# Kernel optimization log

Hardware: AMD Instinct MI355X
Metric: run time of the kernel (lower is better)

## Reference

```python
import jax, jax.numpy as jnp
import numpy as np

B = 4096
FEATURES = 4608 + 4608 + 8 + 1  # 9225
LSTM = 512
R = FEATURES / LSTM
D1 = int(FEATURES / R ** (1.0 / 3.0))
D2 = int(FEATURES / R ** (2.0 / 3.0))
ACTION_SHAPES = (64, 64, 64, 64, 64, 64, 64, 64)


def setup_inputs() -> dict:
    key = jax.random.key(0)
    ks = jax.random.split(key, 32)
    s = 0.02
    inp = {
        "actualCanvasFeatures": jax.random.normal(ks[0], (B, 4608), jnp.float32),
        "objectiveCanvasFeatures": jax.random.normal(ks[1], (B, 4608), jnp.float32),
        "last_action": jax.random.uniform(ks[2], (B, 8), jnp.float32),
        "episode_percentage": 0,
        # encoder MLP
        "W1": jax.random.normal(ks[3], (FEATURES, D1), jnp.float32) * s,
        "b1": jnp.zeros((D1,), jnp.float32),
        "W2": jax.random.normal(ks[4], (D1, D2), jnp.float32) * s,
        "b2": jnp.zeros((D2,), jnp.float32),
        "W3": jax.random.normal(ks[5], (D2, LSTM), jnp.float32) * s,
        "b3": jnp.zeros((LSTM,), jnp.float32),
        # LSTM (torch gate order i,f,g,o)
        "Wih": jax.random.normal(ks[6], (4 * LSTM, LSTM), jnp.float32) * s,
        "Whh": jax.random.normal(ks[7], (4 * LSTM, LSTM), jnp.float32) * s,
        "bih": jnp.zeros((4 * LSTM,), jnp.float32),
        "bhh": jnp.zeros((4 * LSTM,), jnp.float32),
        "h0": jnp.zeros((B, LSTM), jnp.float32),
        "c0": jnp.zeros((B, LSTM), jnp.float32),
        # decoder
        "dW1": jax.random.normal(ks[8], (LSTM, LSTM // 2), jnp.float32) * s,
        "db1": jnp.zeros((LSTM // 2,), jnp.float32),
        "headWs": tuple(jax.random.normal(ks[9 + i], (LSTM // 2, a), jnp.float32) * s
                        for i, a in enumerate(ACTION_SHAPES)),
        "headbs": tuple(jnp.zeros((a,), jnp.float32) for a in ACTION_SHAPES),
        "dWo": jax.random.normal(ks[20], (LSTM + 1, LSTM), jnp.float32) * s,
        "dbo": jnp.zeros((LSTM,), jnp.float32),
    }
    return inp


def reference(actualCanvasFeatures, objectiveCanvasFeatures, last_action,
              episode_percentage, W1, b1, W2, b2, W3, b3, Wih, Whh, bih, bhh,
              h0, c0, dW1, db1, headWs, headbs, dWo, dbo):
    b = actualCanvasFeatures.shape[0]
    ep = jnp.full((b, 1), episode_percentage, dtype=jnp.float32)
    feats = jnp.concatenate(
        [actualCanvasFeatures, objectiveCanvasFeatures, last_action, ep], axis=1)
    # encoder MLP (dropout is eval-mode identity)
    x = jax.nn.relu(feats @ W1 + b1)
    x = jax.nn.relu(x @ W2 + b2)
    x = jax.nn.relu(x @ W3 + b3)
    # single-step LSTM cell, torch gate order i,f,g,o
    gates = x @ Wih.T + bih + h0 @ Whh.T + bhh
    i, f, g, o = jnp.split(gates, 4, axis=1)
    c = jax.nn.sigmoid(f) * c0 + jax.nn.sigmoid(i) * jnp.tanh(g)
    z = jax.nn.sigmoid(o) * jnp.tanh(c)  # seed
    key = jax.random.key(42)
    actions = []
    log_probabilities = jnp.zeros((b,), jnp.float32)
    entropy = jnp.float32(0.0)
    for Wk, bk in zip(headWs, headbs):
        z1 = jax.nn.relu(z @ dW1 + db1)
        logits = z1 @ Wk + bk
        logp = jax.nn.log_softmax(logits, axis=1)
        probs = jnp.exp(logp)
        key, sk = jax.random.split(key)
        act = jax.random.categorical(sk, logits, axis=1)  # [b] int
        actions.append(act.astype(jnp.float32))
        entropy = entropy + jnp.sum(-jnp.sum(probs * logp, axis=1))
        log_probabilities = log_probabilities + jnp.take_along_axis(
            logp, act[:, None], axis=1)[:, 0]
        z = jax.nn.relu(
            jnp.concatenate([z, act.astype(jnp.float32)[:, None]], axis=1) @ dWo + dbo)
    action = jnp.stack(actions, axis=1)  # [b, n_sub_actions]
    return action, entropy, log_probabilities
```

## Files before the change

kernel.cpp:

```cpp
#include <hip/hip_runtime.h>
#include <cstdint>
#include <cstring>

typedef _Float16 f16;
typedef _Float16 f16x8 __attribute__((ext_vector_type(8)));
typedef float f32x4 __attribute__((ext_vector_type(4)));

static constexpr int kPartitionable = 1;

__host__ __device__ inline void tf2x32(uint32_t k0, uint32_t k1,
                                       uint32_t x0, uint32_t x1,
                                       uint32_t& o0, uint32_t& o1) {
  uint32_t ks[3] = {k0, k1, k0 ^ k1 ^ 0x1BD11BDAu};
  uint32_t v0 = x0 + ks[0], v1 = x1 + ks[1];
  const int r0[4] = {13, 15, 26, 6};
  const int r1[4] = {17, 29, 16, 24};
  for (int g = 0; g < 5; ++g) {
    const int* rr = (g & 1) ? r1 : r0;
    for (int j = 0; j < 4; ++j) {
      v0 += v1;
      v1 = (v1 << rr[j]) | (v1 >> (32 - rr[j]));
      v1 ^= v0;
    }
    v0 += ks[(g + 1) % 3];
    v1 += ks[(g + 2) % 3] + (uint32_t)(g + 1);
  }
  o0 = v0; o1 = v1;
}

template <int BM, int BN>
__global__ __launch_bounds__(256, 2) void gemm_split(
    const f16* __restrict__ Ah, const f16* __restrict__ Al, int lda,
    const f16* __restrict__ Bh, const f16* __restrict__ Bl, int ldb,
    int K,
    const float* __restrict__ bias1, const float* __restrict__ bias2,
    int nReal, int relu, int writeF32,
    float* __restrict__ outF, f16* __restrict__ outH, f16* __restrict__ outL,
    int ldo) {
  constexpr int BK = 64;
  constexpr int BKP = BK + 8;
  constexpr int TM = BM / 32;
  constexpr int TN = BN / 32;
  static_assert(BM == BN, "square tiles only");
  __shared__ f16 sAh[BM * BKP];
  __shared__ f16 sAl[BM * BKP];
  __shared__ f16 sBh[BN * BKP];
  __shared__ f16 sBl[BN * BKP];

  const int tid = threadIdx.x;
  const int wave = tid >> 6;
  const int lane = tid & 63;
  const int wm = wave & 1, wn = wave >> 1;
  const int m0 = blockIdx.x * BM;
  const int n0 = blockIdx.y * BN;

  f32x4 acc[TM][TN];
  const f32x4 zero = {0.f, 0.f, 0.f, 0.f};
#pragma unroll
  for (int i = 0; i < TM; ++i)
#pragma unroll
    for (int j = 0; j < TN; ++j) acc[i][j] = zero;

  const f16* src;
  f16* dst;
  int ld, base;
  if (wave == 0)      { src = Ah; dst = sAh; ld = lda; base = m0; }
  else if (wave == 1) { src = Al; dst = sAl; ld = lda; base = m0; }
  else if (wave == 2) { src = Bh; dst = sBh; ld = ldb; base = n0; }
  else                { src = Bl; dst = sBl; ld = ldb; base = n0; }
  constexpr int NITER = (BM * 8) / 64;

  for (int k0 = 0; k0 < K; k0 += BK) {
    __syncthreads();
#pragma unroll
    for (int j = 0; j < NITER; ++j) {
      int c = j * 64 + lane;
      int row = c >> 3, col = c & 7;
      const uint4* g = (const uint4*)(src + (size_t)(base + row) * ld + k0) + col;
      uint4 v = *g;
      ((uint4*)dst)[row * 9 + col] = v;
    }
    __syncthreads();
#pragma unroll
    for (int kk = 0; kk < BK; kk += 32) {
      const int fr = lane & 15;
      const int q8 = (lane >> 4) * 8;
      f16x8 aH[TM], aL[TM], bH[TN], bL[TN];
#pragma unroll
      for (int i = 0; i < TM; ++i) {
        int off = (wm * (BM / 2) + i * 16 + fr) * BKP + kk + q8;
        aH[i] = *(const f16x8*)&sAh[off];
        aL[i] = *(const f16x8*)&sAl[off];
      }
#pragma unroll
      for (int j = 0; j < TN; ++j) {
        int off = (wn * (BN / 2) + j * 16 + fr) * BKP + kk + q8;
        bH[j] = *(const f16x8*)&sBh[off];
        bL[j] = *(const f16x8*)&sBl[off];
      }
#pragma unroll
      for (int i = 0; i < TM; ++i)
#pragma unroll
        for (int j = 0; j < TN; ++j) {
          acc[i][j] = __builtin_amdgcn_mfma_f32_16x16x32_f16(aH[i], bH[j], acc[i][j], 0, 0, 0);
          acc[i][j] = __builtin_amdgcn_mfma_f32_16x16x32_f16(aH[i], bL[j], acc[i][j], 0, 0, 0);
          acc[i][j] = __builtin_amdgcn_mfma_f32_16x16x32_f16(aL[i], bH[j], acc[i][j], 0, 0, 0);
        }
    }
  }
  const int rq = lane >> 4, cl = lane & 15;
#pragma unroll
  for (int i = 0; i < TM; ++i)
#pragma unroll
    for (int j = 0; j < TN; ++j)
#pragma unroll
      for (int r = 0; r < 4; ++r) {
        int row = m0 + wm * (BM / 2) + i * 16 + rq * 4 + r;
        int col = n0 + wn * (BN / 2) + j * 16 + cl;
        float v = acc[i][j][r];
        if (col < nReal) {
          if (bias1) v += bias1[col];
          if (bias2) v += bias2[col];
          if (relu) v = fmaxf(v, 0.f);
        } else {
          v = 0.f;
        }
        size_t o = (size_t)row * ldo + col;
        if (writeF32) {
          outF[o] = v;
        } else {
          f16 h = (f16)v;
          outH[o] = h;
          outL[o] = (f16)(v - (float)h);
        }
      }
}

__global__ void conv_feats(const float* __restrict__ A, const float* __restrict__ O,
                           const float* __restrict__ LA, const int* __restrict__ EP,
                           f16* __restrict__ H, f16* __restrict__ L) {
  uint32_t idx = blockIdx.x * 256u + threadIdx.x;
  const uint32_t total = 4096u * 9280u;
  if (idx >= total) return;
  uint32_t b = idx / 9280u, c = idx - b * 9280u;
  float v;
  if (c < 4608u) v = A[(size_t)b * 4608 + c];
  else if (c < 9216u) v = O[(size_t)b * 4608 + (c - 4608u)];
  else if (c < 9224u) v = LA[(size_t)b * 8 + (c - 9216u)];
  else if (c == 9224u) v = (float)EP[0];
  else v = 0.f;
  f16 h = (f16)v;
  H[idx] = h;
  L[idx] = (f16)(v - (float)h);
}

__global__ void convT_kernel(const float* __restrict__ W, int Kreal, int Nreal,
                             f16* __restrict__ BtH, f16* __restrict__ BtL, int Kpad) {
  __shared__ float tile[32][33];
  int k0 = blockIdx.x * 32, n0 = blockIdx.y * 32;
  int tx = threadIdx.x, ty = threadIdx.y;
  for (int r = 0; r < 32; r += 8) {
    int k = k0 + ty + r, n = n0 + tx;
    float v = (k < Kreal && n < Nreal) ? W[(size_t)k * Nreal + n] : 0.f;
    tile[ty + r][tx] = v;
  }
  __syncthreads();
  for (int r = 0; r < 32; r += 8) {
    int n = n0 + ty + r, k = k0 + tx;
    float v = tile[tx][ty + r];
    size_t o = (size_t)n * Kpad + k;
    f16 h = (f16)v;
    BtH[o] = h;
    BtL[o] = (f16)(v - (float)h);
  }
}

__global__ void conv_lstmB(const float* __restrict__ Wih, const float* __restrict__ Whh,
                           f16* __restrict__ H, f16* __restrict__ L) {
  uint32_t idx = blockIdx.x * 256u + threadIdx.x;
  uint32_t n = idx >> 10, k = idx & 1023u;
  float v = (k < 512u) ? Wih[(size_t)n * 512 + k] : Whh[(size_t)n * 512 + (k - 512u)];
  f16 h = (f16)v;
  H[idx] = h;
  L[idx] = (f16)(v - (float)h);
}

__global__ void conv_h0(const float* __restrict__ h0, f16* __restrict__ H, f16* __restrict__ L) {
  uint32_t idx = blockIdx.x * 256u + threadIdx.x;
  uint32_t b = idx >> 9, j = idx & 511u;
  float v = h0[idx];
  size_t o = (size_t)b * 1024 + 512 + j;
  f16 h = (f16)v;
  H[o] = h;
  L[o] = (f16)(v - (float)h);
}

__global__ void lstm_pointwise(const float* __restrict__ gates, const float* __restrict__ c0,
                               f16* __restrict__ zH, f16* __restrict__ zL) {
  uint32_t idx = blockIdx.x * 256u + threadIdx.x;
  uint32_t b = idx >> 9, n = idx & 511u;
  const float* g = gates + (size_t)b * 2048;
  float gi = g[n], gf = g[512 + n], gg = g[1024 + n], go = g[1536 + n];
  float si = 1.f / (1.f + expf(-gi));
  float sf = 1.f / (1.f + expf(-gf));
  float so = 1.f / (1.f + expf(-go));
  float c = sf * c0[idx] + si * tanhf(gg);
  float z = so * tanhf(c);
  size_t o = (size_t)b * 576 + n;
  f16 h = (f16)z;
  zH[o] = h;
  zL[o] = (f16)(z - (float)h);
}

__global__ void init_ws(f16* zAH, f16* zAL, f16* zBH, f16* zBL,
                        float* wsLogp, float* wsEnt) {
  uint32_t idx = blockIdx.x * 256u + threadIdx.x;
  if (idx < 4096u * 63u) {
    uint32_t b = idx / 63u, c = 513u + idx - b * 63u;
    size_t o = (size_t)b * 576 + c;
    zAH[o] = (f16)0.f; zAL[o] = (f16)0.f; zBH[o] = (f16)0.f; zBL[o] = (f16)0.f;
  }
  if (idx < 4096u) wsLogp[idx] = 0.f;
  if (idx == 0) *wsEnt = 0.f;
}

__device__ inline double shfl_xor_dbl(double v, int m) {
  union { double d; int i[2]; } u;
  u.d = v;
  u.i[0] = __shfl_xor(u.i[0], m);
  u.i[1] = __shfl_xor(u.i[1], m);
  return u.d;
}

__global__ void sample_head(const float* __restrict__ logits,
                            uint32_t sk0, uint32_t sk1, int head, int partitionable,
                            float* __restrict__ outAct,
                            f16* __restrict__ zH, f16* __restrict__ zL,
                            float* __restrict__ wsLogp, float* __restrict__ wsEnt) {
  int wave = threadIdx.x >> 6, lane = threadIdx.x & 63;
  int b = blockIdx.x * 4 + wave;
  float l = logits[(size_t)b * 128 + lane];

  uint32_t i = (uint32_t)b * 64u + (uint32_t)lane;
  uint32_t bits;
  if (partitionable) {
    uint32_t o0, o1;
    tf2x32(sk0, sk1, 0u, i, o0, o1);
    bits = o0 ^ o1;
  } else {
    const uint32_t H = 131072u;
    uint32_t c0, c1, o0, o1;
    int pick;
    if (i < H) { c0 = i; c1 = i + H; pick = 0; }
    else       { c0 = i - H; c1 = i; pick = 1; }
    tf2x32(sk0, sk1, c0, c1, o0, o1);
    bits = pick ? o1 : o0;
  }
  uint32_t ub = (bits >> 9) | 0x3f800000u;
  float u;
  __builtin_memcpy(&u, &ub, 4);
  u -= 1.0f;
  if (u == 0.0f) u = 1.17549435e-38f;
  double gum = -log(-log((double)u));
  double s = (double)l + gum;

  int bi = lane;
  double bv = s;
#pragma unroll
  for (int off = 1; off < 64; off <<= 1) {
    double ov = shfl_xor_dbl(bv, off);
    int oi = __shfl_xor(bi, off);
    if (ov > bv || (ov == bv && oi < bi)) { bv = ov; bi = oi; }
  }
  int act = bi;

  float m = l;
#pragma unroll
  for (int off = 1; off < 64; off <<= 1) m = fmaxf(m, __shfl_xor(m, off));
  float e = expf(l - m);
  float S = e, D = e * l;
#pragma unroll
  for (int off = 1; off < 64; off <<= 1) {
    S += __shfl_xor(S, off);
    D += __shfl_xor(D, off);
  }
  float M = m + logf(S);
  float Hrow = M - D / S;
  float l_act = __shfl(l, act);

  if (lane == 0) {
    outAct[(size_t)b * 8 + head] = (float)act;
    wsLogp[b] += (l_act - M);
    size_t zo = (size_t)b * 576 + 512;
    zH[zo] = (f16)act;
    zL[zo] = (f16)0.f;
  }
  __shared__ float hs[4];
  if (lane == 0) hs[wave] = Hrow;
  __syncthreads();
  if (threadIdx.x == 0) atomicAdd(wsEnt, hs[0] + hs[1] + hs[2] + hs[3]);
}

__global__ void finalize_out(const float* __restrict__ wsEnt, const float* __restrict__ wsLogp,
                             float* __restrict__ out) {
  uint32_t idx = blockIdx.x * 256u + threadIdx.x;
  if (idx == 0) out[32768] = *wsEnt;
  if (idx < 4096u) out[32769 + idx] = wsLogp[idx];
}

extern "C" void kernel_launch(void* const* d_in, const int* in_sizes, int n_in,
                              void* d_out, int out_size, void* d_ws, size_t ws_size,
                              hipStream_t stream) {
  (void)in_sizes; (void)out_size; (void)ws_size;
  const float* actual = (const float*)d_in[0];
  const float* object = (const float*)d_in[1];
  const float* lastA = (const float*)d_in[2];
  const int* ep = (const int*)d_in[3];
  const float* W1 = (const float*)d_in[4];
  const float* b1 = (const float*)d_in[5];
  const float* W2 = (const float*)d_in[6];
  const float* b2 = (const float*)d_in[7];
  const float* W3 = (const float*)d_in[8];
  const float* b3 = (const float*)d_in[9];
  const float* Wih = (const float*)d_in[10];
  const float* Whh = (const float*)d_in[11];
  const float* bih = (const float*)d_in[12];
  const float* bhh = (const float*)d_in[13];
  const float* h0 = (const float*)d_in[14];
  const float* c0 = (const float*)d_in[15];
  const float* dW1 = (const float*)d_in[16];
  const float* db1 = (const float*)d_in[17];
  const float* headW[8];
  const float* headb[8];
  const float *dWo, *dbo;
  if (n_in >= 36) {
    for (int h = 0; h < 8; ++h) headW[h] = (const float*)d_in[18 + h];
    for (int h = 0; h < 8; ++h) headb[h] = (const float*)d_in[26 + h];
    dWo = (const float*)d_in[34];
    dbo = (const float*)d_in[35];
  } else {
    const float* hw = (const float*)d_in[18];
    const float* hb = (const float*)d_in[19];
    for (int h = 0; h < 8; ++h) { headW[h] = hw + (size_t)h * 256 * 64; headb[h] = hb + (size_t)h * 64; }
    dWo = (const float*)d_in[20];
    dbo = (const float*)d_in[21];
  }

  constexpr int Bq = 4096;
  constexpr int K1 = 9280, N1 = 3584, N1r = 3518;
  constexpr int K2 = 3584, N2 = 1408, N2r = 1342;
  constexpr int K3 = 1408, N3 = 512;
  constexpr int KL = 1024, NL = 2048;
  constexpr int KD1 = 512, ND1 = 256;
  constexpr int KH = 256, NHp = 128;
  constexpr int KDO = 576, NDO = 512;

  uint8_t* w = (uint8_t*)d_ws;
  size_t off = 0;
  auto alloc = [&](size_t bytes) -> void* {
    off = (off + 1023) & ~(size_t)1023;
    void* p = w + off;
    off += bytes;
    return p;
  };
  f16* A1h = (f16*)alloc((size_t)Bq * K1 * 2);
  f16* A1l = (f16*)alloc((size_t)Bq * K1 * 2);
  size_t fixedReuseEnd = off;
  f16* Bt1h = (f16*)alloc((size_t)N1 * K1 * 2);
  f16* Bt1l = (f16*)alloc((size_t)N1 * K1 * 2);
  f16* x1h = (f16*)alloc((size_t)Bq * K2 * 2);
  f16* x1l = (f16*)alloc((size_t)Bq * K2 * 2);
  f16* Bt2h = (f16*)alloc((size_t)N2 * K2 * 2);
  f16* Bt2l = (f16*)alloc((size_t)N2 * K2 * 2);
  size_t poff = 0;
  auto palloc = [&](size_t bytes) -> void* {
    poff = (poff + 1023) & ~(size_t)1023;
    void* p = w + poff;
    poff += bytes;
    return p;
  };
  f16* x2h = (f16*)palloc((size_t)Bq * K3 * 2);
  f16* x2l = (f16*)palloc((size_t)Bq * K3 * 2);
  f16* Bt3h = (f16*)palloc((size_t)N3 * K3 * 2);
  f16* Bt3l = (f16*)palloc((size_t)N3 * K3 * 2);
  f16* ALh = (f16*)palloc((size_t)Bq * KL * 2);
  f16* ALl = (f16*)palloc((size_t)Bq * KL * 2);
  f16* BLh = (f16*)palloc((size_t)NL * KL * 2);
  f16* BLl = (f16*)palloc((size_t)NL * KL * 2);
  float* gates = (float*)palloc((size_t)Bq * NL * 4);
  f16* zAH = (f16*)palloc((size_t)Bq * 576 * 2);
  f16* zAL = (f16*)palloc((size_t)Bq * 576 * 2);
  f16* zBH = (f16*)palloc((size_t)Bq * 576 * 2);
  f16* zBL = (f16*)palloc((size_t)Bq * 576 * 2);
  f16* Btd1h = (f16*)palloc((size_t)ND1 * KD1 * 2);
  f16* Btd1l = (f16*)palloc((size_t)ND1 * KD1 * 2);
  f16* z1h = (f16*)palloc((size_t)Bq * ND1 * 2);
  f16* z1l = (f16*)palloc((size_t)Bq * ND1 * 2);
  f16* Bthh = (f16*)palloc((size_t)8 * NHp * KH * 2);
  f16* Bthl = (f16*)palloc((size_t)8 * NHp * KH * 2);
  float* logitsF = (float*)palloc((size_t)Bq * 128 * 4);
  f16* Btdoh = (f16*)palloc((size_t)NDO * KDO * 2);
  f16* Btdol = (f16*)palloc((size_t)NDO * KDO * 2);
  float* wsLogp = (float*)palloc((size_t)Bq * 4);
  float* wsEnt = (float*)palloc(64);
  (void)fixedReuseEnd;

  uint32_t k0 = 0u, k1 = 42u;
  uint32_t sk[8][2];
  for (int h = 0; h < 8; ++h) {
    if (kPartitionable) {
      uint32_t a0, a1, b0v, b1v;
      tf2x32(k0, k1, 0u, 0u, a0, a1);
      tf2x32(k0, k1, 0u, 1u, b0v, b1v);
      sk[h][0] = b0v; sk[h][1] = b1v;
      k0 = a0; k1 = a1;
    } else {
      uint32_t a0, a1, b0v, b1v;
      tf2x32(k0, k1, 0u, 2u, a0, a1);
      tf2x32(k0, k1, 1u, 3u, b0v, b1v);
      sk[h][0] = a1; sk[h][1] = b1v;
      k0 = a0; k1 = b0v;
    }
  }

  dim3 blk(256);
  dim3 tblk(32, 8);

  conv_feats<<<(4096u * 9280u + 255) / 256, blk, 0, stream>>>(actual, object, lastA, ep, A1h, A1l);
  convT_kernel<<<dim3(K1 / 32, N1 / 32), tblk, 0, stream>>>(W1, 9225, 3518, Bt1h, Bt1l, K1);
  convT_kernel<<<dim3(K2 / 32, N2 / 32), tblk, 0, stream>>>(W2, 3518, 1342, Bt2h, Bt2l, K2);

  gemm_split<128, 128><<<dim3(Bq / 128, N1 / 128), blk, 0, stream>>>(
      A1h, A1l, K1, Bt1h, Bt1l, K1, K1, b1, nullptr, N1r, 1, 0, nullptr, x1h, x1l, K2);

  init_ws<<<(4096u * 63u + 255) / 256, blk, 0, stream>>>(zAH, zAL, zBH, zBL, wsLogp, wsEnt);
  convT_kernel<<<dim3(K3 / 32, N3 / 32), tblk, 0, stream>>>(W3, 1342, 512, Bt3h, Bt3l, K3);
  conv_lstmB<<<(2048u * 1024u) / 256, blk, 0, stream>>>(Wih, Whh, BLh, BLl);
  conv_h0<<<(4096u * 512u) / 256, blk, 0, stream>>>(h0, ALh, ALl);
  convT_kernel<<<dim3(KD1 / 32, ND1 / 32), tblk, 0, stream>>>(dW1, 512, 256, Btd1h, Btd1l, KD1);
  convT_kernel<<<dim3(KDO / 32, NDO / 32), tblk, 0, stream>>>(dWo, 513, 512, Btdoh, Btdol, KDO);
  for (int h = 0; h < 8; ++h)
    convT_kernel<<<dim3(KH / 32, NHp / 32), tblk, 0, stream>>>(
        headW[h], 256, 64, Bthh + (size_t)h * NHp * KH, Bthl + (size_t)h * NHp * KH, KH);

  gemm_split<128, 128><<<dim3(Bq / 128, N2 / 128), blk, 0, stream>>>(
      x1h, x1l, K2, Bt2h, Bt2l, K2, K2, b2, nullptr, N2r, 1, 0, nullptr, x2h, x2l, K3);
  gemm_split<128, 128><<<dim3(Bq / 128, N3 / 128), blk, 0, stream>>>(
      x2h, x2l, K3, Bt3h, Bt3l, K3, K3, b3, nullptr, N3, 1, 0, nullptr, ALh, ALl, KL);
  gemm_split<128, 128><<<dim3(Bq / 128, NL / 128), blk, 0, stream>>>(
      ALh, ALl, KL, BLh, BLl, KL, KL, bih, bhh, NL, 0, 1, gates, nullptr, nullptr, NL);
  lstm_pointwise<<<(4096u * 512u) / 256, blk, 0, stream>>>(gates, c0, zAH, zAL);

  for (int h = 0; h < 8; ++h) {
    f16* curH = (h & 1) ? zBH : zAH;
    f16* curL = (h & 1) ? zBL : zAL;
    f16* nxtH = (h & 1) ? zAH : zBH;
    f16* nxtL = (h & 1) ? zAL : zBL;
    gemm_split<64, 64><<<dim3(Bq / 64, ND1 / 64), blk, 0, stream>>>(
        curH, curL, 576, Btd1h, Btd1l, KD1, KD1, db1, nullptr, ND1, 1, 0, nullptr, z1h, z1l, ND1);
    gemm_split<64, 64><<<dim3(Bq / 64, NHp / 64), blk, 0, stream>>>(
        z1h, z1l, ND1, Bthh + (size_t)h * NHp * KH, Bthl + (size_t)h * NHp * KH, KH, KH,
        headb[h], nullptr, 64, 0, 1, logitsF, nullptr, nullptr, 128);
    sample_head<<<Bq / 4, blk, 0, stream>>>(logitsF, sk[h][0], sk[h][1], h, kPartitionable,
                                            (float*)d_out, curH, curL, wsLogp, wsEnt);
    gemm_split<64, 64><<<dim3(Bq / 64, NDO / 64), blk, 0, stream>>>(
        curH, curL, 576, Btdoh, Btdol, KDO, KDO, dbo, nullptr, NDO, 1, 0, nullptr, nxtH, nxtL, 576);
  }
  finalize_out<<<(4097 + 255) / 256, blk, 0, stream>>>(wsEnt, wsLogp, (float*)d_out);
}
```

Before: 2.024 ms.

## Fuse autoregressive decoder loop into one persistent kernel with LDS-resident state

Replaces the 8-head decoder loop of 32 separate GEMM and sampling launches plus finalize with a single kernel, where each 16-row block keeps z, z1 and logits in shared memory across all heads. It also merges the eight head-weight transposes into one launch and drops the workspace init and finalize kernels. The aim is to remove launch overhead and global round-trips for the intermediate activations. The cost is that only 256 blocks run, each with small 16-row MFMA tiles that read weights directly from global memory without LDS staging, so the kernel may be latency-bound and have low occupancy.

```diff
diff --git a/kernel.cpp b/kernel.cpp
--- a/kernel.cpp
+++ b/kernel.cpp
@@ -7,6 +7,9 @@
 typedef float f32x4 __attribute__((ext_vector_type(4)));
 
 static constexpr int kPartitionable = 1;
+
+struct Ptr8 { const float* p[8]; };
+struct Keys8 { uint32_t k[8][2]; };
 
 __host__ __device__ inline void tf2x32(uint32_t k0, uint32_t k1,
                                        uint32_t x0, uint32_t x1,
@@ -175,6 +178,29 @@
   }
 }
 
+__global__ void convT_heads(Ptr8 ws, f16* __restrict__ BtH, f16* __restrict__ BtL) {
+  __shared__ float tile[32][33];
+  int h = blockIdx.z;
+  const float* W = ws.p[h];
+  int k0 = blockIdx.x * 32, n0 = blockIdx.y * 32;
+  int tx = threadIdx.x, ty = threadIdx.y;
+  for (int r = 0; r < 32; r += 8) {
+    int k = k0 + ty + r, n = n0 + tx;
+    float v = (k < 256 && n < 64) ? W[(size_t)k * 64 + n] : 0.f;
+    tile[ty + r][tx] = v;
+  }
+  __syncthreads();
+  size_t base = (size_t)h * 64 * 256;
+  for (int r = 0; r < 32; r += 8) {
+    int n = n0 + ty + r, k = k0 + tx;
+    float v = tile[tx][ty + r];
+    size_t o = base + (size_t)n * 256 + k;
+    f16 hh = (f16)v;
+    BtH[o] = hh;
+    BtL[o] = (f16)(v - (float)hh);
+  }
+}
+
 __global__ void conv_lstmB(const float* __restrict__ Wih, const float* __restrict__ Whh,
                            f16* __restrict__ H, f16* __restrict__ L) {
   uint32_t idx = blockIdx.x * 256u + threadIdx.x;
@@ -206,22 +232,13 @@
   float so = 1.f / (1.f + expf(-go));
   float c = sf * c0[idx] + si * tanhf(gg);
   float z = so * tanhf(c);
-  size_t o = (size_t)b * 576 + n;
   f16 h = (f16)z;
-  zH[o] = h;
-  zL[o] = (f16)(z - (float)h);
-}
-
-__global__ void init_ws(f16* zAH, f16* zAL, f16* zBH, f16* zBL,
-                        float* wsLogp, float* wsEnt) {
-  uint32_t idx = blockIdx.x * 256u + threadIdx.x;
-  if (idx < 4096u * 63u) {
-    uint32_t b = idx / 63u, c = 513u + idx - b * 63u;
-    size_t o = (size_t)b * 576 + c;
-    zAH[o] = (f16)0.f; zAL[o] = (f16)0.f; zBH[o] = (f16)0.f; zBL[o] = (f16)0.f;
-  }
-  if (idx < 4096u) wsLogp[idx] = 0.f;
-  if (idx == 0) *wsEnt = 0.f;
+  zH[idx] = h;
+  zL[idx] = (f16)(z - (float)h);
+}
+
+__global__ void init_ent(float* __restrict__ out) {
+  if (threadIdx.x == 0 && blockIdx.x == 0) out[32768] = 0.f;
 }
 
 __device__ inline double shfl_xor_dbl(double v, int m) {
@@ -232,80 +249,194 @@
   return u.d;
 }
 
-__global__ void sample_head(const float* __restrict__ logits,
-                            uint32_t sk0, uint32_t sk1, int head, int partitionable,
-                            float* __restrict__ outAct,
-                            f16* __restrict__ zH, f16* __restrict__ zL,
-                            float* __restrict__ wsLogp, float* __restrict__ wsEnt) {
-  int wave = threadIdx.x >> 6, lane = threadIdx.x & 63;
-  int b = blockIdx.x * 4 + wave;
-  float l = logits[(size_t)b * 128 + lane];
-
-  uint32_t i = (uint32_t)b * 64u + (uint32_t)lane;
-  uint32_t bits;
-  if (partitionable) {
-    uint32_t o0, o1;
-    tf2x32(sk0, sk1, 0u, i, o0, o1);
-    bits = o0 ^ o1;
-  } else {
-    const uint32_t H = 131072u;
-    uint32_t c0, c1, o0, o1;
-    int pick;
-    if (i < H) { c0 = i; c1 = i + H; pick = 0; }
-    else       { c0 = i - H; c1 = i; pick = 1; }
-    tf2x32(sk0, sk1, c0, c1, o0, o1);
-    bits = pick ? o1 : o0;
-  }
-  uint32_t ub = (bits >> 9) | 0x3f800000u;
-  float u;
-  __builtin_memcpy(&u, &ub, 4);
-  u -= 1.0f;
-  if (u == 0.0f) u = 1.17549435e-38f;
-  double gum = -log(-log((double)u));
-  double s = (double)l + gum;
-
-  int bi = lane;
-  double bv = s;
-#pragma unroll
-  for (int off = 1; off < 64; off <<= 1) {
-    double ov = shfl_xor_dbl(bv, off);
-    int oi = __shfl_xor(bi, off);
-    if (ov > bv || (ov == bv && oi < bi)) { bv = ov; bi = oi; }
-  }
-  int act = bi;
-
-  float m = l;
-#pragma unroll
-  for (int off = 1; off < 64; off <<= 1) m = fmaxf(m, __shfl_xor(m, off));
-  float e = expf(l - m);
-  float S = e, D = e * l;
-#pragma unroll
-  for (int off = 1; off < 64; off <<= 1) {
-    S += __shfl_xor(S, off);
-    D += __shfl_xor(D, off);
-  }
-  float M = m + logf(S);
-  float Hrow = M - D / S;
-  float l_act = __shfl(l, act);
-
-  if (lane == 0) {
-    outAct[(size_t)b * 8 + head] = (float)act;
-    wsLogp[b] += (l_act - M);
-    size_t zo = (size_t)b * 576 + 512;
-    zH[zo] = (f16)act;
-    zL[zo] = (f16)0.f;
-  }
-  __shared__ float hs[4];
-  if (lane == 0) hs[wave] = Hrow;
+__global__ __launch_bounds__(256, 2) void decoder_fused(
+    const f16* __restrict__ zH0, const f16* __restrict__ zL0,
+    const f16* __restrict__ Bd1H, const f16* __restrict__ Bd1L,
+    const float* __restrict__ db1,
+    const f16* __restrict__ BhH, const f16* __restrict__ BhL,
+    Ptr8 hb,
+    const f16* __restrict__ BdoH, const f16* __restrict__ BdoL,
+    const float* __restrict__ dbo,
+    Keys8 sk, int partitionable,
+    float* __restrict__ out) {
+  constexpr int ZS = 584;
+  constexpr int Z1S = 264;
+  __shared__ f16 zbH[16 * ZS], zbL[16 * ZS];
+  __shared__ f16 z1H[16 * Z1S], z1L[16 * Z1S];
+  __shared__ float lgt[16 * 64];
+  __shared__ float entSh[4];
+
+  const int tid = threadIdx.x;
+  const int wave = tid >> 6, lane = tid & 63;
+  const int fr = lane & 15, rq = lane >> 4;
+  const int q8 = rq * 8;
+  const int rowG0 = blockIdx.x * 16;
+  const f32x4 zero = {0.f, 0.f, 0.f, 0.f};
+
+#pragma unroll
+  for (int t = 0; t < 4; ++t) {
+    int ch = t * 256 + tid;
+    int r = ch >> 6, c8 = (ch & 63) * 8;
+    *(f16x8*)&zbH[r * ZS + c8] = *(const f16x8*)&zH0[(size_t)(rowG0 + r) * 512 + c8];
+    *(f16x8*)&zbL[r * ZS + c8] = *(const f16x8*)&zL0[(size_t)(rowG0 + r) * 512 + c8];
+  }
+  if (tid < 128) {
+    int r = tid >> 3, c8 = 512 + (tid & 7) * 8;
+    f16x8 zz = {0, 0, 0, 0, 0, 0, 0, 0};
+    *(f16x8*)&zbH[r * ZS + c8] = zz;
+    *(f16x8*)&zbL[r * ZS + c8] = zz;
+  }
+
+  float entAcc = 0.f;
+  float logpAcc[4] = {0.f, 0.f, 0.f, 0.f};
+
+  for (int h = 0; h < 8; ++h) {
+    __syncthreads();
+    {
+      f32x4 acc[4];
+#pragma unroll
+      for (int j = 0; j < 4; ++j) acc[j] = zero;
+      for (int k0 = 0; k0 < 512; k0 += 32) {
+        f16x8 aH = *(const f16x8*)&zbH[fr * ZS + k0 + q8];
+        f16x8 aL = *(const f16x8*)&zbL[fr * ZS + k0 + q8];
+#pragma unroll
+        for (int j = 0; j < 4; ++j) {
+          int n = wave * 64 + j * 16 + fr;
+          f16x8 bH = *(const f16x8*)&Bd1H[n * 512 + k0 + q8];
+          f16x8 bL = *(const f16x8*)&Bd1L[n * 512 + k0 + q8];
+          acc[j] = __builtin_amdgcn_mfma_f32_16x16x32_f16(aH, bH, acc[j], 0, 0, 0);
+          acc[j] = __builtin_amdgcn_mfma_f32_16x16x32_f16(aH, bL, acc[j], 0, 0, 0);
+          acc[j] = __builtin_amdgcn_mfma_f32_16x16x32_f16(aL, bH, acc[j], 0, 0, 0);
+        }
+      }
+#pragma unroll
+      for (int j = 0; j < 4; ++j) {
+        int col = wave * 64 + j * 16 + fr;
+        float bb = db1[col];
+#pragma unroll
+        for (int r = 0; r < 4; ++r) {
+          float v = fmaxf(acc[j][r] + bb, 0.f);
+          int row = rq * 4 + r;
+          f16 hv = (f16)v;
+          z1H[row * Z1S + col] = hv;
+          z1L[row * Z1S + col] = (f16)(v - (float)hv);
+        }
+      }
+    }
+    __syncthreads();
+    {
+      f32x4 acc = zero;
+      const f16* BH = BhH + (size_t)h * 64 * 256;
+      const f16* BL = BhL + (size_t)h * 64 * 256;
+      int n = wave * 16 + fr;
+      for (int k0 = 0; k0 < 256; k0 += 32) {
+        f16x8 aH = *(const f16x8*)&z1H[fr * Z1S + k0 + q8];
+        f16x8 aL = *(const f16x8*)&z1L[fr * Z1S + k0 + q8];
+        f16x8 bH = *(const f16x8*)&BH[n * 256 + k0 + q8];
+        f16x8 bL = *(const f16x8*)&BL[n * 256 + k0 + q8];
+        acc = __builtin_amdgcn_mfma_f32_16x16x32_f16(aH, bH, acc, 0, 0, 0);
+        acc = __builtin_amdgcn_mfma_f32_16x16x32_f16(aH, bL, acc, 0, 0, 0);
+        acc = __builtin_amdgcn_mfma_f32_16x16x32_f16(aL, bH, acc, 0, 0, 0);
+      }
+      float bb = hb.p[h][n];
+#pragma unroll
+      for (int r = 0; r < 4; ++r) lgt[(rq * 4 + r) * 64 + n] = acc[r] + bb;
+    }
+    __syncthreads();
+    for (int rr = 0; rr < 4; ++rr) {
+      int row = wave * 4 + rr;
+      int b = rowG0 + row;
+      float l = lgt[row * 64 + lane];
+      uint32_t i = (uint32_t)b * 64u + (uint32_t)lane;
+      uint32_t bits;
+      if (partitionable) {
+        uint32_t o0, o1;
+        tf2x32(sk.k[h][0], sk.k[h][1], 0u, i, o0, o1);
+        bits = o0 ^ o1;
+      } else {
+        const uint32_t Hh = 131072u;
+        uint32_t c0, c1, o0, o1;
+        int pick;
+        if (i < Hh) { c0 = i; c1 = i + Hh; pick = 0; }
+        else        { c0 = i - Hh; c1 = i; pick = 1; }
+        tf2x32(sk.k[h][0], sk.k[h][1], c0, c1, o0, o1);
+        bits = pick ? o1 : o0;
+      }
+      uint32_t ub = (bits >> 9) | 0x3f800000u;
+      float u;
+      __builtin_memcpy(&u, &ub, 4);
+      u -= 1.0f;
+      if (u == 0.0f) u = 1.17549435e-38f;
+      double gum = -log(-log((double)u));
+      double s = (double)l + gum;
+      int bi = lane;
+      double bv = s;
+#pragma unroll
+      for (int off = 1; off < 64; off <<= 1) {
+        double ov = shfl_xor_dbl(bv, off);
+        int oi = __shfl_xor(bi, off);
+        if (ov > bv || (ov == bv && oi < bi)) { bv = ov; bi = oi; }
+      }
+      int act = bi;
+      float m = l;
+#pragma unroll
+      for (int off = 1; off < 64; off <<= 1) m = fmaxf(m, __shfl_xor(m, off));
+      float e = expf(l - m);
+      float S = e, D = e * l;
+#pragma unroll
+      for (int off = 1; off < 64; off <<= 1) {
+        S += __shfl_xor(S, off);
+        D += __shfl_xor(D, off);
+      }
+      float M = m + logf(S);
+      entAcc += (M - D / S);
+      float l_act = __shfl(l, act);
+      logpAcc[rr] += (l_act - M);
+      if (lane == 0) {
+        out[(size_t)b * 8 + h] = (float)act;
+        zbH[row * ZS + 512] = (f16)act;
+        zbL[row * ZS + 512] = (f16)0.f;
+      }
+    }
+    __syncthreads();
+    {
+      f32x4 accD[8];
+#pragma unroll
+      for (int j = 0; j < 8; ++j) accD[j] = zero;
+      for (int k0 = 0; k0 < 576; k0 += 32) {
+        f16x8 aH = *(const f16x8*)&zbH[fr * ZS + k0 + q8];
+        f16x8 aL = *(const f16x8*)&zbL[fr * ZS + k0 + q8];
+#pragma unroll
+        for (int j = 0; j < 8; ++j) {
+          int n = wave * 128 + j * 16 + fr;
+          f16x8 bH = *(const f16x8*)&BdoH[n * 576 + k0 + q8];
+          f16x8 bL = *(const f16x8*)&BdoL[n * 576 + k0 + q8];
+          accD[j] = __builtin_amdgcn_mfma_f32_16x16x32_f16(aH, bH, accD[j], 0, 0, 0);
+          accD[j] = __builtin_amdgcn_mfma_f32_16x16x32_f16(aH, bL, accD[j], 0, 0, 0);
+          accD[j] = __builtin_amdgcn_mfma_f32_16x16x32_f16(aL, bH, accD[j], 0, 0, 0);
+        }
+      }
+      __syncthreads();
+#pragma unroll
+      for (int j = 0; j < 8; ++j) {
+        int col = wave * 128 + j * 16 + fr;
+        float bb = dbo[col];
+#pragma unroll
+        for (int r = 0; r < 4; ++r) {
+          float v = fmaxf(accD[j][r] + bb, 0.f);
+          int row = rq * 4 + r;
+          f16 hv = (f16)v;
+          zbH[row * ZS + col] = hv;
+          zbL[row * ZS + col] = (f16)(v - (float)hv);
+        }
+      }
+    }
+  }
+  if (lane == 0) entSh[wave] = entAcc;
   __syncthreads();
-  if (threadIdx.x == 0) atomicAdd(wsEnt, hs[0] + hs[1] + hs[2] + hs[3]);
-}
-
-__global__ void finalize_out(const float* __restrict__ wsEnt, const float* __restrict__ wsLogp,
-                             float* __restrict__ out) {
-  uint32_t idx = blockIdx.x * 256u + threadIdx.x;
-  if (idx == 0) out[32768] = *wsEnt;
-  if (idx < 4096u) out[32769 + idx] = wsLogp[idx];
+  if (tid == 0) atomicAdd(&out[32768], entSh[0] + entSh[1] + entSh[2] + entSh[3]);
+  if (lane == 0)
+    for (int rr = 0; rr < 4; ++rr) out[32769 + rowG0 + wave * 4 + rr] = logpAcc[rr];
 }
 
 extern "C" void kernel_launch(void* const* d_in, const int* in_sizes, int n_in,
@@ -340,8 +471,8 @@
     dbo = (const float*)d_in[35];
   } else {
     const float* hw = (const float*)d_in[18];
-    const float* hb = (const float*)d_in[19];
-    for (int h = 0; h < 8; ++h) { headW[h] = hw + (size_t)h * 256 * 64; headb[h] = hb + (size_t)h * 64; }
+    const float* hbp = (const float*)d_in[19];
+    for (int h = 0; h < 8; ++h) { headW[h] = hw + (size_t)h * 256 * 64; headb[h] = hbp + (size_t)h * 64; }
     dWo = (const float*)d_in[20];
     dbo = (const float*)d_in[21];
   }
@@ -352,7 +483,7 @@
   constexpr int K3 = 1408, N3 = 512;
   constexpr int KL = 1024, NL = 2048;
   constexpr int KD1 = 512, ND1 = 256;
-  constexpr int KH = 256, NHp = 128;
+  constexpr int KH = 256;
   constexpr int KDO = 576, NDO = 512;
 
   uint8_t* w = (uint8_t*)d_ws;
@@ -365,7 +496,6 @@
   };
   f16* A1h = (f16*)alloc((size_t)Bq * K1 * 2);
   f16* A1l = (f16*)alloc((size_t)Bq * K1 * 2);
-  size_t fixedReuseEnd = off;
   f16* Bt1h = (f16*)alloc((size_t)N1 * K1 * 2);
   f16* Bt1l = (f16*)alloc((size_t)N1 * K1 * 2);
   f16* x1h = (f16*)alloc((size_t)Bq * K2 * 2);
@@ -388,40 +518,34 @@
   f16* BLh = (f16*)palloc((size_t)NL * KL * 2);
   f16* BLl = (f16*)palloc((size_t)NL * KL * 2);
   float* gates = (float*)palloc((size_t)Bq * NL * 4);
-  f16* zAH = (f16*)palloc((size_t)Bq * 576 * 2);
-  f16* zAL = (f16*)palloc((size_t)Bq * 576 * 2);
-  f16* zBH = (f16*)palloc((size_t)Bq * 576 * 2);
-  f16* zBL = (f16*)palloc((size_t)Bq * 576 * 2);
+  f16* zAH = (f16*)palloc((size_t)Bq * 512 * 2);
+  f16* zAL = (f16*)palloc((size_t)Bq * 512 * 2);
   f16* Btd1h = (f16*)palloc((size_t)ND1 * KD1 * 2);
   f16* Btd1l = (f16*)palloc((size_t)ND1 * KD1 * 2);
-  f16* z1h = (f16*)palloc((size_t)Bq * ND1 * 2);
-  f16* z1l = (f16*)palloc((size_t)Bq * ND1 * 2);
-  f16* Bthh = (f16*)palloc((size_t)8 * NHp * KH * 2);
-  f16* Bthl = (f16*)palloc((size_t)8 * NHp * KH * 2);
-  float* logitsF = (float*)palloc((size_t)Bq * 128 * 4);
+  f16* Bthh = (f16*)palloc((size_t)8 * 64 * KH * 2);
+  f16* Bthl = (f16*)palloc((size_t)8 * 64 * KH * 2);
   f16* Btdoh = (f16*)palloc((size_t)NDO * KDO * 2);
   f16* Btdol = (f16*)palloc((size_t)NDO * KDO * 2);
-  float* wsLogp = (float*)palloc((size_t)Bq * 4);
-  float* wsEnt = (float*)palloc(64);
-  (void)fixedReuseEnd;
 
   uint32_t k0 = 0u, k1 = 42u;
-  uint32_t sk[8][2];
+  Keys8 sk;
   for (int h = 0; h < 8; ++h) {
     if (kPartitionable) {
       uint32_t a0, a1, b0v, b1v;
       tf2x32(k0, k1, 0u, 0u, a0, a1);
       tf2x32(k0, k1, 0u, 1u, b0v, b1v);
-      sk[h][0] = b0v; sk[h][1] = b1v;
+      sk.k[h][0] = b0v; sk.k[h][1] = b1v;
       k0 = a0; k1 = a1;
     } else {
       uint32_t a0, a1, b0v, b1v;
       tf2x32(k0, k1, 0u, 2u, a0, a1);
       tf2x32(k0, k1, 1u, 3u, b0v, b1v);
-      sk[h][0] = a1; sk[h][1] = b1v;
+      sk.k[h][0] = a1; sk.k[h][1] = b1v;
       k0 = a0; k1 = b0v;
     }
   }
+  Ptr8 hws, hbs;
+  for (int h = 0; h < 8; ++h) { hws.p[h] = headW[h]; hbs.p[h] = headb[h]; }
 
   dim3 blk(256);
   dim3 tblk(32, 8);
@@ -433,15 +557,13 @@
   gemm_split<128, 128><<<dim3(Bq / 128, N1 / 128), blk, 0, stream>>>(
       A1h, A1l, K1, Bt1h, Bt1l, K1, K1, b1, nullptr, N1r, 1, 0, nullptr, x1h, x1l, K2);
 
-  init_ws<<<(4096u * 63u + 255) / 256, blk, 0, stream>>>(zAH, zAL, zBH, zBL, wsLogp, wsEnt);
   convT_kernel<<<dim3(K3 / 32, N3 / 32), tblk, 0, stream>>>(W3, 1342, 512, Bt3h, Bt3l, K3);
   conv_lstmB<<<(2048u * 1024u) / 256, blk, 0, stream>>>(Wih, Whh, BLh, BLl);
   conv_h0<<<(4096u * 512u) / 256, blk, 0, stream>>>(h0, ALh, ALl);
   convT_kernel<<<dim3(KD1 / 32, ND1 / 32), tblk, 0, stream>>>(dW1, 512, 256, Btd1h, Btd1l, KD1);
   convT_kernel<<<dim3(KDO / 32, NDO / 32), tblk, 0, stream>>>(dWo, 513, 512, Btdoh, Btdol, KDO);
-  for (int h = 0; h < 8; ++h)
-    convT_kernel<<<dim3(KH / 32, NHp / 32), tblk, 0, stream>>>(
-        headW[h], 256, 64, Bthh + (size_t)h * NHp * KH, Bthl + (size_t)h * NHp * KH, KH);
+  convT_heads<<<dim3(KH / 32, 2, 8), tblk, 0, stream>>>(hws, Bthh, Bthl);
+  init_ent<<<1, 64, 0, stream>>>((float*)d_out);
 
   gemm_split<128, 128><<<dim3(Bq / 128, N2 / 128), blk, 0, stream>>>(
       x1h, x1l, K2, Bt2h, Bt2l, K2, K2, b2, nullptr, N2r, 1, 0, nullptr, x2h, x2l, K3);
@@ -451,20 +573,7 @@
       ALh, ALl, KL, BLh, BLl, KL, KL, bih, bhh, NL, 0, 1, gates, nullptr, nullptr, NL);
   lstm_pointwise<<<(4096u * 512u) / 256, blk, 0, stream>>>(gates, c0, zAH, zAL);
 
-  for (int h = 0; h < 8; ++h) {
-    f16* curH = (h & 1) ? zBH : zAH;
-    f16* curL = (h & 1) ? zBL : zAL;
-    f16* nxtH = (h & 1) ? zAH : zBH;
-    f16* nxtL = (h & 1) ? zAL : zBL;
-    gemm_split<64, 64><<<dim3(Bq / 64, ND1 / 64), blk, 0, stream>>>(
-        curH, curL, 576, Btd1h, Btd1l, KD1, KD1, db1, nullptr, ND1, 1, 0, nullptr, z1h, z1l, ND1);
-    gemm_split<64, 64><<<dim3(Bq / 64, NHp / 64), blk, 0, stream>>>(
-        z1h, z1l, ND1, Bthh + (size_t)h * NHp * KH, Bthl + (size_t)h * NHp * KH, KH, KH,
-        headb[h], nullptr, 64, 0, 1, logitsF, nullptr, nullptr, 128);
-    sample_head<<<Bq / 4, blk, 0, stream>>>(logitsF, sk[h][0], sk[h][1], h, kPartitionable,
-                                            (float*)d_out, curH, curL, wsLogp, wsEnt);
-    gemm_split<64, 64><<<dim3(Bq / 64, NDO / 64), blk, 0, stream>>>(
-        curH, curL, 576, Btdoh, Btdol, KDO, KDO, dbo, nullptr, NDO, 1, 0, nullptr, nxtH, nxtL, 576);
-  }
-  finalize_out<<<(4097 + 255) / 256, blk, 0, stream>>>(wsEnt, wsLogp, (float*)d_out);
-}
+  decoder_fused<<<256, blk, 0, stream>>>(
+      zAH, zAL, Btd1h, Btd1l, db1, Bthh, Bthl, hbs, Btdoh, Btdol, dbo,
+      sk, kPartitionable, (float*)d_out);
+}
```

New measurement: 2.219 ms. +9.6%, slower.
